# Optimization experiments

Measured on AMD Instinct MI355X. Metric: run time of the kernel, lower is better.

## Reference

```python
import jax, jax.numpy as jnp
import numpy as np

VOCAB = 32000
NUM_STATE = 256
NLABEL = 64
BATCH = 128
MAXLEN = 256
# transition init scale chosen so E[e^2]*S*a^2/3 ~= 1 -> per-step magnitude ~constant
TRANS_A = 0.208


def setup_inputs() -> dict:
    key = jax.random.key(0)
    k1, k2, k3, k4 = jax.random.split(key, 4)
    sentences = jax.random.randint(k1, (BATCH, MAXLEN), 0, VOCAB, dtype=jnp.int64)
    # original init: input.weight ~ U(0.5, 0.5) (constant 0.5). Use U(0.25, 0.75) so the
    # emission stays bounded away from 0 (it is divided by) while not being degenerate.
    emb = jax.random.uniform(k2, (VOCAB, NUM_STATE), minval=0.25, maxval=0.75, dtype=jnp.float32)
    transition = jax.random.uniform(k3, (NUM_STATE, NUM_STATE), minval=-TRANS_A, maxval=TRANS_A, dtype=jnp.float32)
    output = jax.random.uniform(k4, (NUM_STATE, NLABEL), minval=-0.5, maxval=0.5, dtype=jnp.float32)
    return {"sentences": sentences, "emb": emb, "transition": transition, "output": output}


def reference(sentences, emb, transition, output):
    # emission: [maxlen, batch, num_state]
    em = emb[sentences.T]

    def step_fwd(carry, e):  # carry: [B,S]
        nxt = jnp.einsum('ij,bj->bi', transition, carry) * e
        return nxt, nxt

    _, fw_rest = jax.lax.scan(step_fwd, em[0], em[1:])
    forwards = jnp.concatenate([em[:1], fw_rest], axis=0)  # [L,B,S]

    em_rev = em[::-1]

    def step_bwd(carry, e):  # uses transition^T
        nxt = jnp.einsum('ji,bj->bi', transition, carry) * e
        return nxt, nxt

    _, bw_rest = jax.lax.scan(step_bwd, em_rev[0], em_rev[1:])
    backwards = jnp.concatenate([em_rev[:1], bw_rest], axis=0)[::-1]  # time-aligned [L,B,S]

    expected_count = forwards * backwards / em
    score = jnp.einsum('lbs,sn->lbn', expected_count, output)
    return score.transpose(1, 0, 2)  # [batch, maxlen, nlabel]
```

## Files before the change

kernel.cpp:

```cpp
#include <hip/hip_runtime.h>
#include <hip/hip_bf16.h>


typedef _Float16 half8 __attribute__((ext_vector_type(8)));
typedef _Float16 half4 __attribute__((ext_vector_type(4)));
typedef float    f32x4 __attribute__((ext_vector_type(4)));
typedef unsigned long long u64;

#define LL 256
#define BB 128
#define SS 256
#define BT 16
#define RSTR8 67
#define RSTRO 65

static __device__ __forceinline__ f32x4 mfma16f(half8 a, half8 b, f32x4 c) {
  return __builtin_amdgcn_mfma_f32_16x16x32_f16(a, b, c, 0, 0, 0);
}

static __device__ __forceinline__ void lds_barrier() {
  __asm__ __volatile__("s_waitcnt lgkmcnt(0)\n\ts_barrier" ::: "memory");
}

static __device__ __forceinline__ u64 pack4(f32x4 v) {
  union { half4 h; u64 u; } x;
  x.h[0] = (_Float16)v[0];
  x.h[1] = (_Float16)v[1];
  x.h[2] = (_Float16)v[2];
  x.h[3] = (_Float16)v[3];
  return x.u;
}

static __device__ __forceinline__ half8 read_frag_s(const u64* plane, int row,
                                                    int kt, int q, int stride8) {
  const int o = row * stride8 + kt * 8 + q * 2;
  union { u64 u[2]; half8 v; } x;
  x.u[0] = plane[o];
  x.u[1] = plane[o + 1];
  return x.v;
}

__global__ __launch_bounds__(1024, 4)
void hmm_chain(const int* __restrict__ sent, const float* __restrict__ emb,
               const float* __restrict__ T, _Float16* __restrict__ fwh,
               _Float16* __restrict__ gh)
{
  __shared__ u64 s_carry[2][BT * RSTR8];
  __shared__ int s_tok[BT * 257];

  const int tid  = threadIdx.x;
  const int lane = tid & 63;
  const int w    = tid >> 6;
  const int m    = lane & 15;
  const int q    = lane >> 4;

  const int  bid = blockIdx.x;
  const bool fwd = (bid < 8);
  const int  bg0 = (fwd ? bid : bid - 8) * BT;
  _Float16* const obuf = fwd ? fwh : gh;
  const int  st  = 16 * w + 4 * q;

  for (int idx = tid; idx < BT * LL; idx += 1024) {
    int bb = idx >> 8, l2 = idx & 255;
    s_tok[bb * 257 + l2] = sent[(bg0 + bb) * LL + l2];
  }
  __syncthreads();

  half8 a_hi[8];
#pragma unroll
  for (int kt = 0; kt < 8; ++kt) {
    const int r0 = 16 * w + m;
    const int kb = 32 * kt + 8 * q;
    float v[8];
    if (fwd) {
      f32x4 f0 = *(const f32x4*)(T + r0 * 256 + kb);
      f32x4 f1 = *(const f32x4*)(T + r0 * 256 + kb + 4);
#pragma unroll
      for (int j = 0; j < 4; ++j) { v[j] = f0[j]; v[4 + j] = f1[j]; }
    } else {
#pragma unroll
      for (int j = 0; j < 8; ++j) v[j] = T[(kb + j) * 256 + r0];
    }
    half8 hi;
#pragma unroll
    for (int j = 0; j < 8; ++j) hi[j] = (_Float16)v[j];
    a_hi[kt] = hi;
  }

  const int l0 = fwd ? 0 : (LL - 1);
  {
    const int tok0 = s_tok[m * 257 + l0];
    f32x4 e0 = *(const f32x4*)(emb + (size_t)tok0 * 256 + st);
    u64 pc = pack4(e0);
    f32x4 one = 1.0f;
    u64 po = fwd ? pc : pack4(one);
    *(u64*)(obuf + (size_t)(l0 * BB + bg0 + m) * SS + st) = po;
    s_carry[0][m * RSTR8 + 4 * w + q] = pc;
  }

  auto ldem = [&](int su) -> f32x4 {
    su = su < LL ? su : LL - 1;
    const int ln = fwd ? su : (LL - 1) - su;
    const int tk = s_tok[m * 257 + ln];
    return *(const f32x4*)(emb + (size_t)tk * 256 + st);
  };

  f32x4 emr0 = ldem(1);
  f32x4 emr1 = ldem(2);
  f32x4 emr2 = ldem(3);
  __syncthreads();

  auto step = [&](int ss, f32x4& emr) {
    const int l  = fwd ? ss : (LL - 1) - ss;
    const int rb = (ss - 1) & 1, wb = ss & 1;

    const u64* pr = &s_carry[rb][0];
    half8 bfr[8];
#pragma unroll
    for (int kt = 0; kt < 8; ++kt)
      bfr[kt] = read_frag_s(pr, m, kt, q, RSTR8);

    f32x4 em_now = emr;
    emr = ldem(ss + 3);

    f32x4 aA = 0.0f, aB = 0.0f;
#pragma unroll
    for (int kt = 0; kt < 4; ++kt) aA = mfma16f(a_hi[kt], bfr[kt], aA);
#pragma unroll
    for (int kt = 4; kt < 8; ++kt) aB = mfma16f(a_hi[kt], bfr[kt], aB);
    f32x4 v  = aA + aB;
    f32x4 cn = v * em_now;

    u64 p0 = pack4(cn);
    s_carry[wb][m * RSTR8 + 4 * w + q] = p0;
    u64 sv = fwd ? p0 : pack4(v);
    lds_barrier();
    *(u64*)(obuf + (size_t)(l * BB + bg0 + m) * SS + st) = sv;
  };

  for (int s = 1; s < LL; s += 3) {
    step(s + 0, emr0);
    step(s + 1, emr1);
    step(s + 2, emr2);
  }
}

__global__ __launch_bounds__(256, 2)
void hmm_score(const _Float16* __restrict__ fwh, const _Float16* __restrict__ gh,
               const float* __restrict__ outm, float* __restrict__ score)
{
  __shared__ u64 p_pl[64 * RSTR8];
  __shared__ u64 o_pl[64 * RSTRO];

  const int tid  = threadIdx.x;
  const int lane = tid & 63;
  const int w    = tid >> 6;
  const int rh   = w >> 1;
  const int np   = w & 1;
  const int m    = lane & 15;
  const int q    = lane >> 4;
  const int R0   = blockIdx.x * 64;

  {
    _Float16* o_h = (_Float16*)o_pl;
    for (int i = tid; i < 4096; i += 256) {
      f32x4 v = *(const f32x4*)(outm + i * 4);
      int k = i >> 4, n0 = (i & 15) * 4;
#pragma unroll
      for (int r = 0; r < 4; ++r)
        o_h[(n0 + r) * (RSTRO * 4) + k] = (_Float16)v[r];
    }
  }

  for (int idx = tid; idx < 64 * 64; idx += 256) {
    int row = idx >> 6, c = idx & 63;
    union { u64 u; half4 h; } a, b, p;
    a.u = *(const u64*)(fwh + (size_t)(R0 + row) * 256 + c * 4);
    b.u = *(const u64*)(gh  + (size_t)(R0 + row) * 256 + c * 4);
    p.h = a.h * b.h;
    p_pl[row * RSTR8 + c] = p.u;
  }
  lds_barrier();

  f32x4 acc[2][2];
#pragma unroll
  for (int j = 0; j < 2; ++j)
#pragma unroll
    for (int jn = 0; jn < 2; ++jn) acc[j][jn] = 0.0f;

#pragma unroll
  for (int kt = 0; kt < 8; ++kt) {
    half8 of[2];
#pragma unroll
    for (int jn = 0; jn < 2; ++jn)
      of[jn] = read_frag_s(o_pl, 16 * (2 * np + jn) + m, kt, q, RSTRO);
#pragma unroll
    for (int j = 0; j < 2; ++j) {
      half8 pf = read_frag_s(p_pl, 32 * rh + 16 * j + m, kt, q, RSTR8);
#pragma unroll
      for (int jn = 0; jn < 2; ++jn)
        acc[j][jn] = mfma16f(pf, of[jn], acc[j][jn]);
    }
  }

#pragma unroll
  for (int j = 0; j < 2; ++j) {
#pragma unroll
    for (int jn = 0; jn < 2; ++jn) {
#pragma unroll
      for (int r = 0; r < 4; ++r) {
        int row = R0 + 32 * rh + 16 * j + 4 * q + r;
        int l = row >> 7, b = row & 127;
        score[(size_t)b * 16384 + l * 64 + 16 * (2 * np + jn) + m] = acc[j][jn][r];
      }
    }
  }
}

extern "C" void kernel_launch(void* const* d_in, const int* in_sizes, int n_in,
                              void* d_out, int out_size, void* d_ws, size_t ws_size,
                              hipStream_t stream) {
  (void)in_sizes; (void)n_in; (void)out_size; (void)ws_size;
  const int*   sent = (const int*)d_in[0];
  const float* emb  = (const float*)d_in[1];
  const float* T    = (const float*)d_in[2];
  const float* outm = (const float*)d_in[3];
  _Float16* fwh = (_Float16*)d_ws;
  _Float16* gh  = fwh + (size_t)LL * BB * SS;

  hmm_chain<<<16, 1024, 0, stream>>>(sent, emb, T, fwh, gh);
  hmm_score<<<512, 256, 0, stream>>>(fwh, gh, outm, (float*)d_out);
}
```

Baseline: 301.5 us.

## Halve chain block to 8 waves, each computing two 16-row state tiles

The recurrent chain kernel now runs 512 threads (8 waves) instead of 16 waves, and each wave computes two 16-row output tiles that share the same B fragments from the carry buffer. K-tile order is rotated for odd waves to spread LDS bank accesses, and fragment reads are interleaved with MFMAs. The aim is a cheaper per-step barrier and fewer LDS reads per MFMA on the latency-bound serial recurrence. The cost is more registers per wave (two sets of A fragments) and twice the serial MFMA work per wave each step.

```diff
diff --git a/kernel.cpp b/kernel.cpp
--- a/kernel.cpp
+++ b/kernel.cpp
@@ -40,7 +40,7 @@
   return x.v;
 }
 
-__global__ __launch_bounds__(1024, 4)
+__global__ __launch_bounds__(512, 2)
 void hmm_chain(const int* __restrict__ sent, const float* __restrict__ emb,
                const float* __restrict__ T, _Float16* __restrict__ fwh,
                _Float16* __restrict__ gh)
@@ -53,95 +53,126 @@
   const int w    = tid >> 6;
   const int m    = lane & 15;
   const int q    = lane >> 4;
+  const int rot  = (w & 1) << 2;
 
   const int  bid = blockIdx.x;
   const bool fwd = (bid < 8);
   const int  bg0 = (fwd ? bid : bid - 8) * BT;
   _Float16* const obuf = fwd ? fwh : gh;
-  const int  st  = 16 * w + 4 * q;
-
-  for (int idx = tid; idx < BT * LL; idx += 1024) {
+
+  for (int idx = tid; idx < BT * LL; idx += 512) {
     int bb = idx >> 8, l2 = idx & 255;
     s_tok[bb * 257 + l2] = sent[(bg0 + bb) * LL + l2];
   }
   __syncthreads();
 
-  half8 a_hi[8];
-#pragma unroll
-  for (int kt = 0; kt < 8; ++kt) {
-    const int r0 = 16 * w + m;
-    const int kb = 32 * kt + 8 * q;
-    float v[8];
-    if (fwd) {
-      f32x4 f0 = *(const f32x4*)(T + r0 * 256 + kb);
-      f32x4 f1 = *(const f32x4*)(T + r0 * 256 + kb + 4);
-#pragma unroll
-      for (int j = 0; j < 4; ++j) { v[j] = f0[j]; v[4 + j] = f1[j]; }
-    } else {
-#pragma unroll
-      for (int j = 0; j < 8; ++j) v[j] = T[(kb + j) * 256 + r0];
-    }
-    half8 hi;
-#pragma unroll
-    for (int j = 0; j < 8; ++j) hi[j] = (_Float16)v[j];
-    a_hi[kt] = hi;
+  half8 a_hi[2][8];
+#pragma unroll
+  for (int t = 0; t < 2; ++t) {
+    const int r0 = 32 * w + 16 * t + m;
+#pragma unroll
+    for (int i = 0; i < 8; ++i) {
+      const int kb = 32 * (i ^ rot) + 8 * q;
+      float v[8];
+      if (fwd) {
+        f32x4 f0 = *(const f32x4*)(T + r0 * 256 + kb);
+        f32x4 f1 = *(const f32x4*)(T + r0 * 256 + kb + 4);
+#pragma unroll
+        for (int j = 0; j < 4; ++j) { v[j] = f0[j]; v[4 + j] = f1[j]; }
+      } else {
+#pragma unroll
+        for (int j = 0; j < 8; ++j) v[j] = T[(kb + j) * 256 + r0];
+      }
+      half8 hi;
+#pragma unroll
+      for (int j = 0; j < 8; ++j) hi[j] = (_Float16)v[j];
+      a_hi[t][i] = hi;
+    }
   }
 
   const int l0 = fwd ? 0 : (LL - 1);
   {
     const int tok0 = s_tok[m * 257 + l0];
-    f32x4 e0 = *(const f32x4*)(emb + (size_t)tok0 * 256 + st);
-    u64 pc = pack4(e0);
     f32x4 one = 1.0f;
-    u64 po = fwd ? pc : pack4(one);
-    *(u64*)(obuf + (size_t)(l0 * BB + bg0 + m) * SS + st) = po;
-    s_carry[0][m * RSTR8 + 4 * w + q] = pc;
-  }
-
-  auto ldem = [&](int su) -> f32x4 {
+    const u64 pone = pack4(one);
+#pragma unroll
+    for (int t = 0; t < 2; ++t) {
+      const int st = 32 * w + 16 * t + 4 * q;
+      f32x4 e0 = *(const f32x4*)(emb + (size_t)tok0 * 256 + st);
+      u64 pc = pack4(e0);
+      u64 po = fwd ? pc : pone;
+      *(u64*)(obuf + (size_t)(l0 * BB + bg0 + m) * SS + st) = po;
+      s_carry[0][m * RSTR8 + 8 * w + 4 * t + q] = pc;
+    }
+  }
+
+  auto ldem = [&](int su, int t) -> f32x4 {
     su = su < LL ? su : LL - 1;
     const int ln = fwd ? su : (LL - 1) - su;
     const int tk = s_tok[m * 257 + ln];
-    return *(const f32x4*)(emb + (size_t)tk * 256 + st);
+    return *(const f32x4*)(emb + (size_t)tk * 256 + 32 * w + 16 * t + 4 * q);
   };
 
-  f32x4 emr0 = ldem(1);
-  f32x4 emr1 = ldem(2);
-  f32x4 emr2 = ldem(3);
+  f32x4 em0a = ldem(1, 0), em0b = ldem(1, 1);
+  f32x4 em1a = ldem(2, 0), em1b = ldem(2, 1);
+  f32x4 em2a = ldem(3, 0), em2b = ldem(3, 1);
   __syncthreads();
 
-  auto step = [&](int ss, f32x4& emr) {
+  auto step = [&](int ss, f32x4& ea, f32x4& eb) {
     const int l  = fwd ? ss : (LL - 1) - ss;
     const int rb = (ss - 1) & 1, wb = ss & 1;
 
     const u64* pr = &s_carry[rb][0];
-    half8 bfr[8];
-#pragma unroll
-    for (int kt = 0; kt < 8; ++kt)
-      bfr[kt] = read_frag_s(pr, m, kt, q, RSTR8);
-
-    f32x4 em_now = emr;
-    emr = ldem(ss + 3);
-
-    f32x4 aA = 0.0f, aB = 0.0f;
-#pragma unroll
-    for (int kt = 0; kt < 4; ++kt) aA = mfma16f(a_hi[kt], bfr[kt], aA);
-#pragma unroll
-    for (int kt = 4; kt < 8; ++kt) aB = mfma16f(a_hi[kt], bfr[kt], aB);
-    f32x4 v  = aA + aB;
-    f32x4 cn = v * em_now;
-
-    u64 p0 = pack4(cn);
-    s_carry[wb][m * RSTR8 + 4 * w + q] = p0;
-    u64 sv = fwd ? p0 : pack4(v);
+    half8 b0 = read_frag_s(pr, m, 0 ^ rot, q, RSTR8);
+    half8 b1 = read_frag_s(pr, m, 1 ^ rot, q, RSTR8);
+    half8 b2 = read_frag_s(pr, m, 2 ^ rot, q, RSTR8);
+    half8 b3 = read_frag_s(pr, m, 3 ^ rot, q, RSTR8);
+
+    f32x4 e0 = ea, e1 = eb;
+    ea = ldem(ss + 3, 0);
+    eb = ldem(ss + 3, 1);
+
+    f32x4 aA0 = 0.0f, aB0 = 0.0f, aA1 = 0.0f, aB1 = 0.0f;
+    aA0 = mfma16f(a_hi[0][0], b0, aA0);
+    aA1 = mfma16f(a_hi[1][0], b0, aA1);
+    b0 = read_frag_s(pr, m, 4 ^ rot, q, RSTR8);
+    aB0 = mfma16f(a_hi[0][1], b1, aB0);
+    aB1 = mfma16f(a_hi[1][1], b1, aB1);
+    b1 = read_frag_s(pr, m, 5 ^ rot, q, RSTR8);
+    aA0 = mfma16f(a_hi[0][2], b2, aA0);
+    aA1 = mfma16f(a_hi[1][2], b2, aA1);
+    b2 = read_frag_s(pr, m, 6 ^ rot, q, RSTR8);
+    aB0 = mfma16f(a_hi[0][3], b3, aB0);
+    aB1 = mfma16f(a_hi[1][3], b3, aB1);
+    b3 = read_frag_s(pr, m, 7 ^ rot, q, RSTR8);
+    aA0 = mfma16f(a_hi[0][4], b0, aA0);
+    aA1 = mfma16f(a_hi[1][4], b0, aA1);
+    aB0 = mfma16f(a_hi[0][5], b1, aB0);
+    aB1 = mfma16f(a_hi[1][5], b1, aB1);
+    aA0 = mfma16f(a_hi[0][6], b2, aA0);
+    aA1 = mfma16f(a_hi[1][6], b2, aA1);
+    aB0 = mfma16f(a_hi[0][7], b3, aB0);
+    aB1 = mfma16f(a_hi[1][7], b3, aB1);
+
+    f32x4 v0 = aA0 + aB0, v1 = aA1 + aB1;
+    f32x4 cn0 = v0 * e0,  cn1 = v1 * e1;
+
+    u64 p0 = pack4(cn0), p1 = pack4(cn1);
+    s_carry[wb][m * RSTR8 + 8 * w + q]     = p0;
+    s_carry[wb][m * RSTR8 + 8 * w + 4 + q] = p1;
+    u64 sv0 = fwd ? p0 : pack4(v0);
+    u64 sv1 = fwd ? p1 : pack4(v1);
     lds_barrier();
-    *(u64*)(obuf + (size_t)(l * BB + bg0 + m) * SS + st) = sv;
+    const int st0 = 32 * w + 4 * q;
+    _Float16* orow = obuf + (size_t)(l * BB + bg0 + m) * SS;
+    *(u64*)(orow + st0)      = sv0;
+    *(u64*)(orow + st0 + 16) = sv1;
   };
 
   for (int s = 1; s < LL; s += 3) {
-    step(s + 0, emr0);
-    step(s + 1, emr1);
-    step(s + 2, emr2);
+    step(s + 0, em0a, em0b);
+    step(s + 1, em1a, em1b);
+    step(s + 2, em2a, em2b);
   }
 }
 
@@ -228,6 +259,6 @@
   _Float16* fwh = (_Float16*)d_ws;
   _Float16* gh  = fwh + (size_t)LL * BB * SS;
 
-  hmm_chain<<<16, 1024, 0, stream>>>(sent, emb, T, fwh, gh);
+  hmm_chain<<<16, 512, 0, stream>>>(sent, emb, T, fwh, gh);
   hmm_score<<<512, 256, 0, stream>>>(fwh, gh, outm, (float*)d_out);
 }
```

After: 301.6 us. About the same (+0.0%).
